# Kernel optimization log

Hardware: AMD Instinct MI355X
Metric: run time of the kernel (lower is better)

Reference implementation:

```python
import jax, jax.numpy as jnp
import numpy as np

EPS = 1e-6

def elu_feature_map(x):
    return jax.nn.elu(x) + 1.0

def setup_inputs() -> dict:
    key = jax.random.key(0)
    ks = jax.random.split(key, 5)
    B, S, D, H, Hd = 4, 4096, 1024, 16, 64
    scale = 1.0 / np.sqrt(D)
    x = jax.random.normal(ks[0], (B, S, D), dtype=jnp.float32)
    Wq = jax.random.normal(ks[1], (D, H, Hd), dtype=jnp.float32) * scale
    Wk = jax.random.normal(ks[2], (D, H, Hd), dtype=jnp.float32) * scale
    Wv = jax.random.normal(ks[3], (D, H, Hd), dtype=jnp.float32) * scale
    Wo = jax.random.normal(ks[4], (H, Hd, D), dtype=jnp.float32) * (1.0 / np.sqrt(H * Hd))
    bq = jnp.zeros((H, Hd), dtype=jnp.float32)
    bk = jnp.zeros((H, Hd), dtype=jnp.float32)
    bv = jnp.zeros((H, Hd), dtype=jnp.float32)
    bo = jnp.zeros((D,), dtype=jnp.float32)
    return {"x": x, "Wq": Wq, "bq": bq, "Wk": Wk, "bk": bk, "Wv": Wv, "bv": bv, "Wo": Wo, "bo": bo}

def reference(x, Wq, bq, Wk, bk, Wv, bv, Wo, bo):
    # QKV projections: [n,s,D] x [D,h,d] -> [n,s,h,d]
    q = jnp.einsum('nsD,Dhd->nshd', x, Wq) + bq
    k = jnp.einsum('nsD,Dhd->nshd', x, Wk) + bk
    v = jnp.einsum('nsD,Dhd->nshd', x, Wv) + bv
    qf = elu_feature_map(q)
    kf = elu_feature_map(k)
    # kv state per head: [n,h,m,d]
    kv = jnp.einsum('nshd,nshm->nhmd', kf, v)
    # normalizer: [n,l,h]
    z = 1.0 / (jnp.einsum('nlhd,nhd->nlh', qf, jnp.sum(kf, axis=1)) + EPS)
    # output: [n,l,h,m]
    y = jnp.einsum('nlhd,nhmd,nlh->nlhm', qf, kv, z)
    # output projection contracting (head, head_dim)
    out = jnp.einsum('nlhm,hmD->nlD', y, Wo) + bo
    return out
```

## Files before the change

kernel.cpp:

```cpp
#include <hip/hip_runtime.h>
#include <cstddef>
#include <cstdint>


typedef __attribute__((ext_vector_type(8))) __bf16 bf16x8;
typedef __attribute__((ext_vector_type(4))) __bf16 bf16x4;
typedef __attribute__((ext_vector_type(2))) __bf16 bf16x2;
typedef __attribute__((ext_vector_type(4))) float f32x4;

__device__ __forceinline__ void async_cp16(const void* g, void* s) {
    __builtin_amdgcn_global_load_lds(
        (__attribute__((address_space(1))) void*)g,
        (__attribute__((address_space(3))) void*)s, 16, 0, 0);
}


#define QUAD(ARR, BRR, RO, CO)                                                 \
    _Pragma("unroll")                                                          \
    for (int _qi = 0; _qi < 4; ++_qi)                                          \
        _Pragma("unroll")                                                      \
        for (int _qj = 0; _qj < 2; ++_qj)                                      \
            _Pragma("unroll")                                                  \
            for (int _qk = 0; _qk < 2; ++_qk)                                  \
                acc[(RO) + _qi][(CO) + _qj] =                                  \
                    __builtin_amdgcn_mfma_f32_16x16x32_bf16(                   \
                        ARR[_qi][_qk], BRR[_qj][_qk],                          \
                        acc[(RO) + _qi][(CO) + _qj], 0, 0, 0);

__device__ __forceinline__ void mfma256_core(const __bf16* __restrict__ A,
                                             const __bf16* __restrict__ BT,
                                             int mbase, int nbase,
                                             f32x4 acc[8][4])
{
    extern __shared__ __bf16 lds[];
    constexpr int NT = 16;
    const int t    = threadIdx.x;
    const int lane = t & 63;
    const int wid  = t >> 6;
    const int wm   = wid >> 2;
    const int wn   = wid & 3;
    const int fr   = lane & 15;
    const int fq   = lane >> 4;
    const int srow  = lane >> 3;
    const int sslot = ((lane & 7) ^ srow) << 3;

    const __bf16* aBase = A  + (size_t)mbase * 1024;
    const __bf16* bBase = BT + (size_t)nbase * 1024;

#define STAGE_A(tile)                                                          \
    { const int _b = (tile) & 1;                                               \
      _Pragma("unroll") for (int _h = 0; _h < 2; ++_h)                         \
      _Pragma("unroll") for (int _i = 0; _i < 2; ++_i) {                       \
          const int _c = 2 * wid + _i;                                         \
          async_cp16(aBase + (size_t)(_h * 128 + _c * 8 + srow) * 1024         \
                         + (tile) * 64 + sslot,                                \
                     lds + _b * 32768 + _h * 8192 + _c * 512); } }
#define STAGE_B(tile)                                                          \
    { const int _b = (tile) & 1;                                               \
      _Pragma("unroll") for (int _h = 0; _h < 2; ++_h)                         \
      _Pragma("unroll") for (int _i = 0; _i < 2; ++_i) {                       \
          const int _c = 2 * wid + _i;                                         \
          async_cp16(bBase + (size_t)(_h * 128 + _c * 8 + srow) * 1024         \
                         + (tile) * 64 + sslot,                                \
                     lds + _b * 32768 + 16384 + _h * 8192 + _c * 512); } }
#define LDA(ri, ks, b)                                                         \
    (*(const bf16x8*)(lds + (b) * 32768 + (wm * 128 + (ri) * 16 + fr) * 64     \
                      + (((ks) * 32 + fq * 8) ^ ((fr & 7) << 3))))
#define LDB(cj, ks, b)                                                         \
    (*(const bf16x8*)(lds + (b) * 32768 + 16384                                \
                      + (wn * 64 + (cj) * 16 + fr) * 64                        \
                      + (((ks) * 32 + fq * 8) ^ ((fr & 7) << 3))))

    bf16x8 aR0[4][2], aR1[4][2], bC0[2][2], bC1[2][2];

    STAGE_A(0) STAGE_B(0) STAGE_A(1) STAGE_B(1)
    asm volatile("s_waitcnt vmcnt(8)" ::: "memory");
    __builtin_amdgcn_s_barrier();

#pragma unroll
    for (int i = 0; i < 4; ++i)
#pragma unroll
        for (int ks = 0; ks < 2; ++ks) aR0[i][ks] = LDA(i, ks, 0);
#pragma unroll
    for (int j = 0; j < 2; ++j)
#pragma unroll
        for (int ks = 0; ks < 2; ++ks) bC0[j][ks] = LDB(j, ks, 0);

    for (int T = 0; T < NT; ++T) {
        const int bc = T & 1, bn = bc ^ 1;

#pragma unroll
        for (int i = 0; i < 4; ++i)
#pragma unroll
            for (int ks = 0; ks < 2; ++ks) aR1[i][ks] = LDA(4 + i, ks, bc);
        __builtin_amdgcn_s_barrier();
        asm volatile("s_waitcnt lgkmcnt(0)" ::: "memory");
        __builtin_amdgcn_sched_barrier(0);
        __builtin_amdgcn_s_setprio(1);
        QUAD(aR0, bC0, 0, 0)
        __builtin_amdgcn_s_setprio(0);
        __builtin_amdgcn_s_barrier();

        asm volatile("s_waitcnt vmcnt(4)" ::: "memory");
#pragma unroll
        for (int j = 0; j < 2; ++j)
#pragma unroll
            for (int ks = 0; ks < 2; ++ks) bC1[j][ks] = LDB(2 + j, ks, bc);
        if (T + 2 < NT) STAGE_A(T + 2)
        __builtin_amdgcn_s_barrier();
        asm volatile("s_waitcnt lgkmcnt(0)" ::: "memory");
        __builtin_amdgcn_sched_barrier(0);
        __builtin_amdgcn_s_setprio(1);
        QUAD(aR0, bC1, 0, 2)
        __builtin_amdgcn_s_setprio(0);
        __builtin_amdgcn_s_barrier();

        asm volatile("s_waitcnt vmcnt(4)" ::: "memory");
        if (T + 1 < NT) {
#pragma unroll
            for (int i = 0; i < 4; ++i)
#pragma unroll
                for (int ks = 0; ks < 2; ++ks) aR0[i][ks] = LDA(i, ks, bn);
        }
        if (T + 2 < NT) STAGE_B(T + 2)
        __builtin_amdgcn_s_barrier();
        asm volatile("s_waitcnt lgkmcnt(0)" ::: "memory");
        __builtin_amdgcn_sched_barrier(0);
        __builtin_amdgcn_s_setprio(1);
        QUAD(aR1, bC0, 4, 0)
        __builtin_amdgcn_s_setprio(0);
        __builtin_amdgcn_s_barrier();

        if (T + 1 < NT) {
#pragma unroll
            for (int j = 0; j < 2; ++j)
#pragma unroll
                for (int ks = 0; ks < 2; ++ks) bC0[j][ks] = LDB(j, ks, bn);
        }
        __builtin_amdgcn_s_barrier();
        asm volatile("s_waitcnt lgkmcnt(0)" ::: "memory");
        __builtin_amdgcn_sched_barrier(0);
        __builtin_amdgcn_s_setprio(1);
        QUAD(aR1, bC1, 4, 2)
        __builtin_amdgcn_s_setprio(0);
        __builtin_amdgcn_s_barrier();
    }
#undef STAGE_A
#undef STAGE_B
#undef LDA
#undef LDB
}

__global__ __launch_bounds__(512) void gemm_qkv_256(
    const __bf16* __restrict__ xb,
    const __bf16* __restrict__ wqt, const __bf16* __restrict__ wkt,
    const __bf16* __restrict__ wvt,
    const float* __restrict__ bq, const float* __restrict__ bk,
    const float* __restrict__ bv,
    __bf16* __restrict__ qfb, __bf16* __restrict__ kfb, __bf16* __restrict__ vb)
{
    f32x4 acc[8][4];
#pragma unroll
    for (int i = 0; i < 8; ++i)
#pragma unroll
        for (int j = 0; j < 4; ++j) acc[i][j] = (f32x4){0.f, 0.f, 0.f, 0.f};

    const int mt = blockIdx.x;
    const int nt = blockIdx.y;
    const int which = nt >> 2;
    const int nbase = (nt & 3) * 256;
    const int mbase = mt * 256;

    const __bf16* BT  = (which == 0) ? wqt : (which == 1) ? wkt : wvt;
    const float* bias = (which == 0) ? bq : (which == 1) ? bk : bv;
    __bf16* outp      = (which == 0) ? qfb : (which == 1) ? kfb : vb;
    const bool feat   = (which < 2);

    mfma256_core(xb, BT, mbase, nbase, acc);

    const int t = threadIdx.x, lane = t & 63, wid = t >> 6;
    const int wm = wid >> 2, wn = wid & 3;
    const int fr = lane & 15, fq = lane >> 4;

#pragma unroll
    for (int ri = 0; ri < 8; ++ri)
#pragma unroll
        for (int cj = 0; cj < 4; ++cj) {
            const int col = nbase + wn * 64 + cj * 16 + fr;
            const float bval = bias[col];
#pragma unroll
            for (int r = 0; r < 4; ++r) {
                const int row = mbase + wm * 128 + ri * 16 + fq * 4 + r;
                float vv = acc[ri][cj][r] + bval;
                if (feat) vv = (vv > 0.f) ? (vv + 1.f) : __expf(vv);
                outp[(size_t)row * 1024 + col] = (__bf16)vv;
            }
        }
}

__global__ __launch_bounds__(512) void gemm_out_256(
    const __bf16* __restrict__ yb, const __bf16* __restrict__ wot,
    const float* __restrict__ bo, float* __restrict__ out)
{
    f32x4 acc[8][4];
#pragma unroll
    for (int i = 0; i < 8; ++i)
#pragma unroll
        for (int j = 0; j < 4; ++j) acc[i][j] = (f32x4){0.f, 0.f, 0.f, 0.f};

    const int mbase = blockIdx.x * 256;
    const int nbase = blockIdx.y * 256;

    mfma256_core(yb, wot, mbase, nbase, acc);

    const int t = threadIdx.x, lane = t & 63, wid = t >> 6;
    const int wm = wid >> 2, wn = wid & 3;
    const int fr = lane & 15, fq = lane >> 4;

#pragma unroll
    for (int ri = 0; ri < 8; ++ri)
#pragma unroll
        for (int cj = 0; cj < 4; ++cj) {
            const int col = nbase + wn * 64 + cj * 16 + fr;
            const float bval = bo[col];
#pragma unroll
            for (int r = 0; r < 4; ++r) {
                const int row = mbase + wm * 128 + ri * 16 + fq * 4 + r;
                out[(size_t)row * 1024 + col] = acc[ri][cj][r] + bval;
            }
        }
}

__global__ __launch_bounds__(256) void kv_ksum_mfma(
    const __bf16* __restrict__ kfb, const __bf16* __restrict__ vb,
    float* __restrict__ kvp, float* __restrict__ ksp)
{
    __shared__ __bf16 kfs[64 * 66];
    __shared__ __bf16 vs[64 * 66];

    const int bh = blockIdx.x;
    const int n = bh >> 4, h = bh & 15;
    const int chunk = blockIdx.y;
    const int t = threadIdx.x, lane = t & 63, w = t >> 6;
    const int fr = lane & 15, fq = lane >> 4;

    f32x4 acc[4];
#pragma unroll
    for (int j = 0; j < 4; j++) acc[j] = (f32x4){0.f, 0.f, 0.f, 0.f};
    f32x4 accks = (f32x4){0.f, 0.f, 0.f, 0.f};

    bf16x8 ones;
#pragma unroll
    for (int e = 0; e < 8; e++) ones[e] = (__bf16)1.0f;

    const size_t base = ((size_t)n * 4096 + (size_t)chunk * 256) * 1024 + h * 64;

    for (int tile = 0; tile < 4; tile++) {
#pragma unroll
        for (int i = 0; i < 2; i++) {
            int idx = t + i * 256;
            int s = idx >> 3, d0 = (idx & 7) * 8;
            bf16x8 k8 = *(const bf16x8*)(kfb + base + (size_t)(tile * 64 + s) * 1024 + d0);
            bf16x8 v8 = *(const bf16x8*)(vb  + base + (size_t)(tile * 64 + s) * 1024 + d0);
#pragma unroll
            for (int e = 0; e < 4; e++) {
                *(bf16x2*)(kfs + s * 66 + d0 + 2 * e) = (bf16x2){k8[2*e], k8[2*e+1]};
                *(bf16x2*)(vs  + s * 66 + d0 + 2 * e) = (bf16x2){v8[2*e], v8[2*e+1]};
            }
        }
        __syncthreads();

#pragma unroll
        for (int kk = 0; kk < 2; kk++) {
            bf16x8 af, bfr[4];
#pragma unroll
            for (int j = 0; j < 8; j++)
                af[j] = vs[(kk * 32 + fq * 8 + j) * 66 + 16 * w + fr];
#pragma unroll
            for (int j2 = 0; j2 < 4; j2++)
#pragma unroll
                for (int j = 0; j < 8; j++)
                    bfr[j2][j] = kfs[(kk * 32 + fq * 8 + j) * 66 + 16 * j2 + fr];
#pragma unroll
            for (int j2 = 0; j2 < 4; j2++)
                acc[j2] = __builtin_amdgcn_mfma_f32_16x16x32_bf16(
                    af, bfr[j2], acc[j2], 0, 0, 0);
            accks = __builtin_amdgcn_mfma_f32_16x16x32_bf16(
                ones, bfr[w], accks, 0, 0, 0);
        }
        __syncthreads();
    }

    const size_t pbase = ((size_t)bh * 16 + chunk) * 4096;
#pragma unroll
    for (int j2 = 0; j2 < 4; j2++)
#pragma unroll
        for (int r = 0; r < 4; r++) {
            int m = 16 * w + fq * 4 + r;
            int d = 16 * j2 + fr;
            kvp[pbase + m * 64 + d] = acc[j2][r];
        }
    if (fq == 0)
        ksp[((size_t)bh * 16 + chunk) * 64 + 16 * w + fr] = accks[0];
}

__global__ __launch_bounds__(256) void reduce_kv(
    const float* __restrict__ kvp, const float* __restrict__ ksp,
    __bf16* __restrict__ kvb, __bf16* __restrict__ ksumb)
{
    const int b = blockIdx.x;
    if (b < 1024) {
        int i = b * 256 + threadIdx.x;
        int bh = i >> 12, md = i & 4095;
        float s = 0.f;
#pragma unroll
        for (int c = 0; c < 16; c++) s += kvp[((size_t)bh * 16 + c) * 4096 + md];
        kvb[i] = (__bf16)s;
    } else {
        int j = (b - 1024) * 256 + threadIdx.x;
        int bh = j >> 6, d = j & 63;
        float s = 0.f;
#pragma unroll
        for (int c = 0; c < 16; c++) s += ksp[((size_t)bh * 16 + c) * 64 + d];
        ksumb[j] = (__bf16)s;
    }
}

__global__ __launch_bounds__(256) void y_mfma(
    const __bf16* __restrict__ qfb, const __bf16* __restrict__ kvb,
    const __bf16* __restrict__ ksumb, __bf16* __restrict__ yb)
{
    __shared__ __bf16 qs[128 * 72];
    __shared__ __bf16 kvs[64 * 72];

    const int gbase = blockIdx.x * 128;
    const int h = blockIdx.y;
    const int bh = (gbase >> 12) * 16 + h;
    const int t = threadIdx.x, lane = t & 63, w = t >> 6;
    const int fr = lane & 15, fq = lane >> 4;

#pragma unroll
    for (int i = 0; i < 4; i++) {
        int idx = t + i * 256;
        int l = idx >> 3, d0 = (idx & 7) * 8;
        *(bf16x8*)(qs + l * 72 + d0) =
            *(const bf16x8*)(qfb + (size_t)(gbase + l) * 1024 + h * 64 + d0);
    }
#pragma unroll
    for (int i = 0; i < 2; i++) {
        int idx = t + i * 256;
        int m = idx >> 3, d0 = (idx & 7) * 8;
        *(bf16x8*)(kvs + m * 72 + d0) =
            *(const bf16x8*)(kvb + (size_t)bh * 4096 + m * 64 + d0);
    }
    bf16x8 ksb[2];
#pragma unroll
    for (int kk = 0; kk < 2; kk++)
        ksb[kk] = *(const bf16x8*)(ksumb + bh * 64 + kk * 32 + fq * 8);
    __syncthreads();

    f32x4 acc[2][4], accz[2];
#pragma unroll
    for (int i = 0; i < 2; i++) {
        accz[i] = (f32x4){0.f, 0.f, 0.f, 0.f};
#pragma unroll
        for (int j = 0; j < 4; j++) acc[i][j] = (f32x4){0.f, 0.f, 0.f, 0.f};
    }

#pragma unroll
    for (int kk = 0; kk < 2; kk++) {
        bf16x8 af[2], bfr[4];
#pragma unroll
        for (int i = 0; i < 2; i++)
            af[i] = *(const bf16x8*)(qs + (32 * w + 16 * i + fr) * 72 + kk * 32 + fq * 8);
#pragma unroll
        for (int j = 0; j < 4; j++)
            bfr[j] = *(const bf16x8*)(kvs + (16 * j + fr) * 72 + kk * 32 + fq * 8);
#pragma unroll
        for (int i = 0; i < 2; i++) {
#pragma unroll
            for (int j = 0; j < 4; j++)
                acc[i][j] = __builtin_amdgcn_mfma_f32_16x16x32_bf16(
                    af[i], bfr[j], acc[i][j], 0, 0, 0);
            accz[i] = __builtin_amdgcn_mfma_f32_16x16x32_bf16(
                af[i], ksb[kk], accz[i], 0, 0, 0);
        }
    }

#pragma unroll
    for (int i = 0; i < 2; i++)
#pragma unroll
        for (int r = 0; r < 4; r++) {
            const float z = 1.0f / (accz[i][r] + 1e-6f);
            const int g = gbase + 32 * w + 16 * i + fq * 4 + r;
#pragma unroll
            for (int j = 0; j < 4; j++)
                yb[(size_t)g * 1024 + h * 64 + 16 * j + fr] =
                    (__bf16)(acc[i][j][r] * z);
        }
}

__global__ __launch_bounds__(256) void cast_x(const float* __restrict__ x,
                                              __bf16* __restrict__ xb)
{
    const size_t i = ((size_t)blockIdx.x * 256 + threadIdx.x) * 8;
    float4 a = *(const float4*)(x + i);
    float4 b = *(const float4*)(x + i + 4);
    bf16x8 o;
    o[0] = (__bf16)a.x; o[1] = (__bf16)a.y; o[2] = (__bf16)a.z; o[3] = (__bf16)a.w;
    o[4] = (__bf16)b.x; o[5] = (__bf16)b.y; o[6] = (__bf16)b.z; o[7] = (__bf16)b.w;
    *(bf16x8*)(xb + i) = o;
}

__global__ __launch_bounds__(256) void transpose_w(
    const float* __restrict__ w0, const float* __restrict__ w1,
    const float* __restrict__ w2, const float* __restrict__ w3,
    __bf16* __restrict__ o0, __bf16* __restrict__ o1,
    __bf16* __restrict__ o2, __bf16* __restrict__ o3)
{
    __shared__ float ld[32][33];
    const int wsel = blockIdx.z;
    const float* src = (wsel == 0) ? w0 : (wsel == 1) ? w1 : (wsel == 2) ? w2 : w3;
    __bf16* dst      = (wsel == 0) ? o0 : (wsel == 1) ? o1 : (wsel == 2) ? o2 : o3;

    const int kbase = blockIdx.x * 32;
    const int nbase = blockIdx.y * 32;
    const int t = threadIdx.x;
    const int r = t >> 3, c4 = (t & 7) * 4;

    float4 a = *(const float4*)(src + (size_t)(kbase + r) * 1024 + nbase + c4);
    ld[r][c4 + 0] = a.x; ld[r][c4 + 1] = a.y; ld[r][c4 + 2] = a.z; ld[r][c4 + 3] = a.w;
    __syncthreads();

    bf16x4 o;
    o[0] = (__bf16)ld[c4 + 0][r];
    o[1] = (__bf16)ld[c4 + 1][r];
    o[2] = (__bf16)ld[c4 + 2][r];
    o[3] = (__bf16)ld[c4 + 3][r];
    *(bf16x4*)(dst + (size_t)(nbase + r) * 1024 + kbase + c4) = o;
}

extern "C" void kernel_launch(void* const* d_in, const int* in_sizes, int n_in,
                              void* d_out, int out_size, void* d_ws, size_t ws_size,
                              hipStream_t stream)
{
    const float* x  = (const float*)d_in[0];
    const float* Wq = (const float*)d_in[1];
    const float* bq = (const float*)d_in[2];
    const float* Wk = (const float*)d_in[3];
    const float* bk = (const float*)d_in[4];
    const float* Wv = (const float*)d_in[5];
    const float* bv = (const float*)d_in[6];
    const float* Wo = (const float*)d_in[7];
    const float* bo = (const float*)d_in[8];
    float* out = (float*)d_out;

    __bf16* xb    = (__bf16*)d_ws;
    __bf16* wqt   = xb + (size_t)16777216;
    __bf16* wkt   = wqt + 1048576;
    __bf16* wvt   = wkt + 1048576;
    __bf16* wot   = wvt + 1048576;
    __bf16* qfb   = wot + 1048576;
    __bf16* kfb   = qfb + (size_t)16777216;
    __bf16* vb    = kfb + (size_t)16777216;
    float*  kvp   = (float*)(vb + (size_t)16777216);
    float*  ksp   = kvp + 4194304;
    __bf16* kvb   = (__bf16*)(ksp + 65536);
    __bf16* ksumb = kvb + 262144;

    const int LDS_BYTES = 131072;
    (void)hipFuncSetAttribute((const void*)gemm_qkv_256,
                              hipFuncAttributeMaxDynamicSharedMemorySize, LDS_BYTES);
    (void)hipFuncSetAttribute((const void*)gemm_out_256,
                              hipFuncAttributeMaxDynamicSharedMemorySize, LDS_BYTES);

    cast_x<<<dim3(8192), dim3(256), 0, stream>>>(x, xb);
    transpose_w<<<dim3(32, 32, 4), dim3(256), 0, stream>>>(
        Wq, Wk, Wv, Wo, wqt, wkt, wvt, wot);

    gemm_qkv_256<<<dim3(64, 12), dim3(512), LDS_BYTES, stream>>>(
        xb, wqt, wkt, wvt, bq, bk, bv, qfb, kfb, vb);
    kv_ksum_mfma<<<dim3(64, 16), dim3(256), 0, stream>>>(kfb, vb, kvp, ksp);
    reduce_kv<<<dim3(1040), dim3(256), 0, stream>>>(kvp, ksp, kvb, ksumb);
    y_mfma<<<dim3(128, 16), dim3(256), 0, stream>>>(qfb, kvb, ksumb, kfb);
    gemm_out_256<<<dim3(64, 4), dim3(512), LDS_BYTES, stream>>>(kfb, wot, bo, out);
}
```

Before: 327.3 us.

## Split GEMM tile staging into halves and stage y output through LDS

The GEMM mainloop now issues global-to-LDS copies in half-tiles spread across the four MFMA phases. It also moves LDS fragment loads ahead of each phase and drops one barrier per phase, so memory traffic overlaps compute more evenly and there is less synchronization stall. Separately, the attention output kernel writes its results into LDS first and then stores 16-byte vectors to global memory instead of scattered 2-byte stores. The risks are harder-to-verify vmcnt accounting that could cause races, and two added __syncthreads in the epilogue.

```diff
diff --git a/kernel.cpp b/kernel.cpp
--- a/kernel.cpp
+++ b/kernel.cpp
@@ -47,22 +47,19 @@
     const __bf16* aBase = A  + (size_t)mbase * 1024;
     const __bf16* bBase = BT + (size_t)nbase * 1024;
 
-#define STAGE_A(tile)                                                          \
-    { const int _b = (tile) & 1;                                               \
-      _Pragma("unroll") for (int _h = 0; _h < 2; ++_h)                         \
-      _Pragma("unroll") for (int _i = 0; _i < 2; ++_i) {                       \
+#define STAGE_AH(tile, hh)                                                     \
+    { _Pragma("unroll") for (int _i = 0; _i < 2; ++_i) {                       \
           const int _c = 2 * wid + _i;                                         \
-          async_cp16(aBase + (size_t)(_h * 128 + _c * 8 + srow) * 1024         \
+          async_cp16(aBase + (size_t)((hh) * 128 + _c * 8 + srow) * 1024       \
                          + (tile) * 64 + sslot,                                \
-                     lds + _b * 32768 + _h * 8192 + _c * 512); } }
-#define STAGE_B(tile)                                                          \
-    { const int _b = (tile) & 1;                                               \
-      _Pragma("unroll") for (int _h = 0; _h < 2; ++_h)                         \
-      _Pragma("unroll") for (int _i = 0; _i < 2; ++_i) {                       \
+                     lds + ((tile) & 1) * 32768 + (hh) * 8192 + _c * 512); } }
+#define STAGE_BH(tile, hh)                                                     \
+    { _Pragma("unroll") for (int _i = 0; _i < 2; ++_i) {                       \
           const int _c = 2 * wid + _i;                                         \
-          async_cp16(bBase + (size_t)(_h * 128 + _c * 8 + srow) * 1024         \
+          async_cp16(bBase + (size_t)((hh) * 128 + _c * 8 + srow) * 1024       \
                          + (tile) * 64 + sslot,                                \
-                     lds + _b * 32768 + 16384 + _h * 8192 + _c * 512); } }
+                     lds + ((tile) & 1) * 32768 + 16384 + (hh) * 8192          \
+                         + _c * 512); } }
 #define LDA(ri, ks, b)                                                         \
     (*(const bf16x8*)(lds + (b) * 32768 + (wm * 128 + (ri) * 16 + fr) * 64     \
                       + (((ks) * 32 + fq * 8) ^ ((fr & 7) << 3))))
@@ -73,8 +70,9 @@
 
     bf16x8 aR0[4][2], aR1[4][2], bC0[2][2], bC1[2][2];
 
-    STAGE_A(0) STAGE_B(0) STAGE_A(1) STAGE_B(1)
-    asm volatile("s_waitcnt vmcnt(8)" ::: "memory");
+    STAGE_AH(0, 0) STAGE_AH(0, 1) STAGE_BH(0, 0) STAGE_BH(0, 1)
+    STAGE_AH(1, 0) STAGE_AH(1, 1) STAGE_BH(1, 0)
+    asm volatile("s_waitcnt vmcnt(6)" ::: "memory");
     __builtin_amdgcn_s_barrier();
 
 #pragma unroll
@@ -93,42 +91,40 @@
         for (int i = 0; i < 4; ++i)
 #pragma unroll
             for (int ks = 0; ks < 2; ++ks) aR1[i][ks] = LDA(4 + i, ks, bc);
-        __builtin_amdgcn_s_barrier();
-        asm volatile("s_waitcnt lgkmcnt(0)" ::: "memory");
+#pragma unroll
+        for (int j = 0; j < 2; ++j)
+#pragma unroll
+            for (int ks = 0; ks < 2; ++ks) bC1[j][ks] = LDB(2 + j, ks, bc);
+        if (T + 1 < NT) STAGE_BH(T + 1, 1)
         __builtin_amdgcn_sched_barrier(0);
         __builtin_amdgcn_s_setprio(1);
         QUAD(aR0, bC0, 0, 0)
         __builtin_amdgcn_s_setprio(0);
+        asm volatile("s_waitcnt lgkmcnt(0)" ::: "memory");
         __builtin_amdgcn_s_barrier();
 
         asm volatile("s_waitcnt vmcnt(4)" ::: "memory");
-#pragma unroll
-        for (int j = 0; j < 2; ++j)
-#pragma unroll
-            for (int ks = 0; ks < 2; ++ks) bC1[j][ks] = LDB(2 + j, ks, bc);
-        if (T + 2 < NT) STAGE_A(T + 2)
-        __builtin_amdgcn_s_barrier();
-        asm volatile("s_waitcnt lgkmcnt(0)" ::: "memory");
+        if (T + 2 < NT) STAGE_AH(T + 2, 0)
         __builtin_amdgcn_sched_barrier(0);
         __builtin_amdgcn_s_setprio(1);
         QUAD(aR0, bC1, 0, 2)
         __builtin_amdgcn_s_setprio(0);
+        asm volatile("s_waitcnt lgkmcnt(0)" ::: "memory");
         __builtin_amdgcn_s_barrier();
 
-        asm volatile("s_waitcnt vmcnt(4)" ::: "memory");
+        asm volatile("s_waitcnt vmcnt(2)" ::: "memory");
         if (T + 1 < NT) {
 #pragma unroll
             for (int i = 0; i < 4; ++i)
 #pragma unroll
                 for (int ks = 0; ks < 2; ++ks) aR0[i][ks] = LDA(i, ks, bn);
         }
-        if (T + 2 < NT) STAGE_B(T + 2)
-        __builtin_amdgcn_s_barrier();
-        asm volatile("s_waitcnt lgkmcnt(0)" ::: "memory");
+        if (T + 2 < NT) STAGE_AH(T + 2, 1)
         __builtin_amdgcn_sched_barrier(0);
         __builtin_amdgcn_s_setprio(1);
         QUAD(aR1, bC0, 4, 0)
         __builtin_amdgcn_s_setprio(0);
+        asm volatile("s_waitcnt lgkmcnt(0)" ::: "memory");
         __builtin_amdgcn_s_barrier();
 
         if (T + 1 < NT) {
@@ -137,16 +133,16 @@
 #pragma unroll
                 for (int ks = 0; ks < 2; ++ks) bC0[j][ks] = LDB(j, ks, bn);
         }
-        __builtin_amdgcn_s_barrier();
-        asm volatile("s_waitcnt lgkmcnt(0)" ::: "memory");
+        if (T + 2 < NT) STAGE_BH(T + 2, 0)
         __builtin_amdgcn_sched_barrier(0);
         __builtin_amdgcn_s_setprio(1);
         QUAD(aR1, bC1, 4, 2)
         __builtin_amdgcn_s_setprio(0);
+        asm volatile("s_waitcnt lgkmcnt(0)" ::: "memory");
         __builtin_amdgcn_s_barrier();
     }
-#undef STAGE_A
-#undef STAGE_B
+#undef STAGE_AH
+#undef STAGE_BH
 #undef LDA
 #undef LDB
 }
@@ -387,17 +383,25 @@
         }
     }
 
+    __syncthreads();
 #pragma unroll
     for (int i = 0; i < 2; i++)
 #pragma unroll
         for (int r = 0; r < 4; r++) {
             const float z = 1.0f / (accz[i][r] + 1e-6f);
-            const int g = gbase + 32 * w + 16 * i + fq * 4 + r;
+            const int lrow = 32 * w + 16 * i + fq * 4 + r;
 #pragma unroll
             for (int j = 0; j < 4; j++)
-                yb[(size_t)g * 1024 + h * 64 + 16 * j + fr] =
-                    (__bf16)(acc[i][j][r] * z);
-        }
+                qs[lrow * 72 + 16 * j + fr] = (__bf16)(acc[i][j][r] * z);
+        }
+    __syncthreads();
+#pragma unroll
+    for (int i = 0; i < 4; i++) {
+        int idx = t + i * 256;
+        int l = idx >> 3, d0 = (idx & 7) * 8;
+        *(bf16x8*)(yb + (size_t)(gbase + l) * 1024 + h * 64 + d0) =
+            *(const bf16x8*)(qs + l * 72 + d0);
+    }
 }
 
 __global__ __launch_bounds__(256) void cast_x(const float* __restrict__ x,
```

Measured after the change: 335.2 us. 2.4% more time.
